# Kernel tuning notes

Measured on AMD Instinct MI355X. Metric: run time of the kernel, lower is better.

Reference implementation:

```python
import jax, jax.numpy as jnp
import numpy as np

B, N, M, H, D = 16, 512, 16, 8, 128  # batch, nodes, neighbors, heads, input_dim
NEG_SLOPE = 0.2
EPS = 1e-5

def _glorot(key, shape):
    fan = sum(shape[-2:]) if len(shape) >= 2 else shape[-1]
    return jax.random.normal(key, shape, dtype=jnp.float32) * (2.0 / fan) ** 0.5

def setup_inputs() -> dict:
    key = jax.random.key(0)
    ks = jax.random.split(key, 12)
    h = jax.random.normal(ks[0], (B, N, D), dtype=jnp.float32)
    adj = jax.random.randint(ks[1], (B, N, M), 0, 2, dtype=jnp.int32)
    n_list = jax.random.randint(ks[2], (B, N, M), 0, N, dtype=jnp.int32)
    W = _glorot(ks[3], (H, D, D))            # per-head projection
    a_src = _glorot(ks[4], (H, D))           # attention vector, source half
    a_dst = _glorot(ks[5], (H, D))           # attention vector, neighbor half
    Wo = _glorot(ks[6], (H * D, D))          # concat-heads output projection
    ln1_g = jnp.ones((D,), jnp.float32); ln1_b = jnp.zeros((D,), jnp.float32)
    ff_w1 = _glorot(ks[7], (D, 2 * D)); ff_b1 = jnp.zeros((2 * D,), jnp.float32)
    ff_w2 = _glorot(ks[8], (2 * D, D)); ff_b2 = jnp.zeros((D,), jnp.float32)
    ln2_g = jnp.ones((D,), jnp.float32); ln2_b = jnp.zeros((D,), jnp.float32)
    return {"h": h, "adj": adj, "n_list": n_list, "W": W, "a_src": a_src,
            "a_dst": a_dst, "Wo": Wo, "ln1_g": ln1_g, "ln1_b": ln1_b,
            "ff_w1": ff_w1, "ff_b1": ff_b1, "ff_w2": ff_w2, "ff_b2": ff_b2,
            "ln2_g": ln2_g, "ln2_b": ln2_b}

def _layer_norm(x, g, b):
    mu = jnp.mean(x, axis=-1, keepdims=True)
    var = jnp.mean(jnp.square(x - mu), axis=-1, keepdims=True)
    return (x - mu) * jax.lax.rsqrt(var + EPS) * g + b

def _gat(h, adj, n_list, W, a_src, a_dst, Wo):
    Wh = jnp.einsum('bnd,hde->bnhe', h, W)                 # [B,N,H,D]
    s_src = jnp.einsum('bnhe,he->bnh', Wh, a_src)          # [B,N,H]
    s_dst = jnp.einsum('bnhe,he->bnh', Wh, a_dst)          # [B,N,H]
    gather = jax.vmap(lambda x, idx: x[idx])               # per-graph gather
    neigh = gather(Wh, n_list)                             # [B,N,M,H,D]
    s_dst_n = gather(s_dst, n_list)                        # [B,N,M,H]
    e = jax.nn.leaky_relu(s_src[:, :, None, :] + s_dst_n, NEG_SLOPE)
    e = jnp.where(adj[..., None] > 0, e, jnp.float32(-1e9))
    attn = jax.nn.softmax(e, axis=2)                       # over M neighbors
    out = jnp.einsum('bnmh,bnmhe->bnhe', attn, neigh)      # [B,N,H,D]
    return out.reshape(out.shape[0], out.shape[1], -1) @ Wo  # [B,N,D]

def reference(h, adj, n_list, W, a_src, a_dst, Wo, ln1_g, ln1_b,
              ff_w1, ff_b1, ff_w2, ff_b2, ln2_g, ln2_b):
    att = _gat(h, adj, n_list, W, a_src, a_dst, Wo)
    t = _layer_norm(att + h, ln1_g, ln1_b)
    ff = jax.nn.relu(t @ ff_w1 + ff_b1) @ ff_w2 + ff_b2
    return _layer_norm(ff + t, ln2_g, ln2_b)
```

## Files before the change

### kernel.cpp

```cpp
#include <hip/hip_runtime.h>
#include <hip/hip_bf16.h>

#define B_  16
#define N_  512
#define M_  16
#define H_  8
#define D_  128
#define BN_ 8192
#define NB  16

typedef __attribute__((ext_vector_type(4))) float          f32x4;
typedef __attribute__((ext_vector_type(4))) _Float16       f16x4;
typedef __attribute__((ext_vector_type(8))) unsigned short u16x8;
typedef __attribute__((ext_vector_type(8))) _Float16       f16x8;

static __device__ __forceinline__ float bf2f(__hip_bfloat16 x) { return __bfloat162float(x); }
static __device__ __forceinline__ unsigned short f2bu(float x) {
    __hip_bfloat16 b = __float2bfloat16(x);
    return *reinterpret_cast<unsigned short*>(&b);
}
static __device__ __forceinline__ float bu2f(unsigned short u) {
    return __uint_as_float(((unsigned int)u) << 16);
}

template <bool F32>
struct Pol {
    static __device__ __forceinline__ float ld(const void* p, int i) {
        if constexpr (F32) return ((const float*)p)[i];
        else               return bf2f(((const __hip_bfloat16*)p)[i]);
    }
    static __device__ __forceinline__ float4 ld4(const void* p, int i) {
        if constexpr (F32) return *(const float4*)((const float*)p + i);
        else {
            const ushort4 u = *(const ushort4*)((const unsigned short*)p + i);
            return make_float4(bu2f(u.x), bu2f(u.y), bu2f(u.z), bu2f(u.w));
        }
    }
    static __device__ __forceinline__ void ld8(const void* p, long i, float* v) {
        if constexpr (F32) {
            const float4 a = *(const float4*)((const float*)p + i);
            const float4 b = *(const float4*)((const float*)p + i + 4);
            v[0]=a.x; v[1]=a.y; v[2]=a.z; v[3]=a.w;
            v[4]=b.x; v[5]=b.y; v[6]=b.z; v[7]=b.w;
        } else {
            const u16x8 u = *(const u16x8*)((const unsigned short*)p + i);
            #pragma unroll
            for (int j = 0; j < 8; ++j) v[j] = bu2f(u[j]);
        }
    }
    static __device__ __forceinline__ void st8(void* p, long i, const float* v) {
        if constexpr (F32) {
            *(float4*)((float*)p + i)     = make_float4(v[0], v[1], v[2], v[3]);
            *(float4*)((float*)p + i + 4) = make_float4(v[4], v[5], v[6], v[7]);
        } else {
            u16x8 u;
            #pragma unroll
            for (int j = 0; j < 8; ++j) u[j] = f2bu(v[j]);
            *(u16x8*)((unsigned short*)p + i) = u;
        }
    }
};

static __device__ __forceinline__ bool probe_is_f32(const void* h) {
    bool is_f32 = false;
    const __hip_bfloat16* hb = (const __hip_bfloat16*)h;
    for (int i = 0; i < 128; ++i) {
        const float v = bf2f(hb[2 * i]);
        if (!(fabsf(v) < 1e4f)) is_f32 = true;
    }
    return is_f32;
}

template <bool F32>
static __device__ __forceinline__ void k0_body(
        const void* __restrict__ W,  const void* __restrict__ Wo,
        const void* __restrict__ a_src, const void* __restrict__ a_dst,
        float* __restrict__ wsrc, float* __restrict__ wdst,
        _Float16* __restrict__ WeffT, float* wrow ) {
    using P = Pol<F32>;
    const int blk = blockIdx.x;
    const int t   = threadIdx.x;
    if (blk < 512) {
        const int half = t >> 7, o = t & 127;
        const int hd = blk * 2 + half;
        wrow[half * 128 + o] = P::ld(W, hd * 128 + o);
        __syncthreads();
        const int hh = hd >> 7;
        float acc = 0.f;
        #pragma unroll 8
        for (int e = 0; e < 128; ++e)
            acc += wrow[half * 128 + e] * P::ld(Wo, (hh * 128 + e) * 128 + o);
        WeffT[(size_t)o * 1024 + hd] = (_Float16)acc;
    } else {
        const int hh = blk - 512;
        const int which = t >> 7, d = t & 127;
        const void* av = which ? a_dst : a_src;
        const int wbase = hh * (D_ * D_) + d * 128;
        float acc = 0.f;
        #pragma unroll 8
        for (int e = 0; e < 128; e += 4) {
            const float4 wv = P::ld4(W, wbase + e);
            const float4 aa = P::ld4(av, hh * 128 + e);
            acc += wv.x * aa.x + wv.y * aa.y + wv.z * aa.z + wv.w * aa.w;
        }
        (which ? wdst : wsrc)[hh * 128 + d] = acc;
    }
}

__global__ __launch_bounds__(256) void k0(
        const void* W, const void* Wo, const void* a_src, const void* a_dst,
        const void* h, float* wsrc, float* wdst, _Float16* WeffT) {
    __shared__ float wrow[2 * 128];
    if (probe_is_f32(h)) k0_body<true >(W, Wo, a_src, a_dst, wsrc, wdst, WeffT, wrow);
    else                 k0_body<false>(W, Wo, a_src, a_dst, wsrc, wdst, WeffT, wrow);
}

template <bool F32>
static __device__ __forceinline__ void k1_body(
        const void* __restrict__ h, const float* __restrict__ wsrc,
        const float* __restrict__ wdst, _Float16* __restrict__ ssrc_h,
        _Float16* __restrict__ sdst_h, float* hls , float* wls ) {
    using P = Pol<F32>;
    const int t   = threadIdx.x;
    const int bn0 = blockIdx.x * 16;
    {
        const int r = t >> 4, c0 = (t & 15) * 8;
        float v[8];
        P::ld8(h, (long)(bn0 + r) * 128 + c0, v);
        #pragma unroll
        for (int j = 0; j < 8; ++j) hls[r * 132 + c0 + j] = v[j];
        const int c = t >> 4;
        const float* wp = (c >> 3) ? wdst : wsrc;
        const int woff = (c & 7) * 128 + c0;
        #pragma unroll
        for (int j = 0; j < 8; ++j) wls[c * 132 + c0 + j] = wp[woff + j];
    }
    __syncthreads();
    const int n = t >> 4, c = t & 15;
    float acc = 0.f;
    #pragma unroll
    for (int e = 0; e < 128; e += 4) {
        const float4 hv = *(const float4*)(hls + n * 132 + e);
        const float4 wv = *(const float4*)(wls + c * 132 + e);
        acc += hv.x * wv.x + hv.y * wv.y + hv.z * wv.z + hv.w * wv.w;
    }
    const int node = bn0 + n;
    if (c < 8) ssrc_h[node * 8 + c]       = (_Float16)acc;
    else       sdst_h[node * 8 + (c - 8)] = (_Float16)acc;
}

__global__ __launch_bounds__(256) void k1(const void* h, const float* wsrc,
                                          const float* wdst, _Float16* ssrc_h,
                                          _Float16* sdst_h) {
    __shared__ float hls[16 * 132];
    __shared__ float wls[16 * 132];
    if (probe_is_f32(h)) k1_body<true >(h, wsrc, wdst, ssrc_h, sdst_h, hls, wls);
    else                 k1_body<false>(h, wsrc, wdst, ssrc_h, sdst_h, hls, wls);
}

struct __align__(16) Smem {
    union {
        _Float16 Zh[NB][1024];
        struct {
            float    ts[NB][132];
            _Float16 us[NB][260];
            float    ys[NB][128];
        } ff;
    } u;
    float hs[NB][128];
    union {
        float attn[NB][16][8];
        float yln[NB][128];
    } v;
    int   nls[NB][16];
    int   adjs[NB][16];
    float ssrc[NB][8];
};

template <bool F32>
static __device__ __forceinline__ void gat_body(
        Smem& s,
        const void* __restrict__ h,
        const int*  __restrict__ adj,
        const int*  __restrict__ n_list,
        const _Float16* __restrict__ ssrc_h,
        const _Float16* __restrict__ sdst_h,
        const _Float16* __restrict__ WeffT,
        const void* __restrict__ g1, const void* __restrict__ bb1,
        const void* __restrict__ w1, const void* __restrict__ fb1,
        const void* __restrict__ w2, const void* __restrict__ fb2,
        const void* __restrict__ g2, const void* __restrict__ bb2,
        void* __restrict__ out) {
    using P = Pol<F32>;
    const int t   = threadIdx.x;
    const int bn0 = blockIdx.x * NB;
    const int b   = bn0 >> 9;
    const int l   = t & 63;
    const int w   = t >> 6;
    const int lo  = l & 15;
    const int hi  = l >> 4;

    {
        const int r = t >> 5, c0 = (t & 31) * 4;
        const float4 v = P::ld4(h, (bn0 + r) * 128 + c0);
        *(float4*)&s.hs[r][c0] = v;
    }
    if (t < 256) {
        const int r = t >> 4, m = t & 15;
        s.nls[r][m]  = n_list[(bn0 + r) * M_ + m] & (N_ - 1);
        s.adjs[r][m] = adj[(bn0 + r) * M_ + m];
    }
    if (t < NB * 8) s.ssrc[t >> 3][t & 7] = (float)ssrc_h[bn0 * 8 + t];
    __syncthreads();

    if (t < 256) {
        const int r = t >> 4, m = t & 15;
        const int nbr = s.nls[r][m];
        const f16x8 sd = *(const f16x8*)(sdst_h + (size_t)(b * N_ + nbr) * 8);
        const int amask = s.adjs[r][m];
        float sc[8];
        #pragma unroll
        for (int hh = 0; hh < 8; ++hh) {
            float x = s.ssrc[r][hh] + (float)sd[hh];
            x = x > 0.f ? x : 0.2f * x;
            if (amask == 0) x = -1e9f;
            sc[hh] = x;
        }
        *(float4*)&s.v.attn[r][m][0] = make_float4(sc[0], sc[1], sc[2], sc[3]);
        *(float4*)&s.v.attn[r][m][4] = make_float4(sc[4], sc[5], sc[6], sc[7]);
    }
    __syncthreads();

    if (t < NB * 8) {
        const int r = t >> 3, hh = t & 7;
        float mx = -3.4e38f;
        #pragma unroll
        for (int m = 0; m < 16; ++m) mx = fmaxf(mx, s.v.attn[r][m][hh]);
        float ex[16], sum = 0.f;
        #pragma unroll
        for (int m = 0; m < 16; ++m) { ex[m] = __expf(s.v.attn[r][m][hh] - mx); sum += ex[m]; }
        const float inv = 1.f / sum;
        #pragma unroll
        for (int m = 0; m < 16; ++m) s.v.attn[r][m][hh] = ex[m] * inv;
    }
    __syncthreads();

    {
        const int r = t >> 5, dc = t & 31, d0 = dc * 4;
        float z[8][4];
        #pragma unroll
        for (int hh = 0; hh < 8; ++hh)
            #pragma unroll
            for (int jj = 0; jj < 4; ++jj) z[hh][jj] = 0.f;
        #pragma unroll 4
        for (int m = 0; m < 16; ++m) {
            const int nbr = s.nls[r][m];
            const float4 hv = P::ld4(h, (b * N_ + nbr) * 128 + d0);
            const float hv4[4] = { hv.x, hv.y, hv.z, hv.w };
            const float4 a0 = *(const float4*)&s.v.attn[r][m][0];
            const float4 a1 = *(const float4*)&s.v.attn[r][m][4];
            const float av[8] = { a0.x, a0.y, a0.z, a0.w, a1.x, a1.y, a1.z, a1.w };
            #pragma unroll
            for (int hh = 0; hh < 8; ++hh)
                #pragma unroll
                for (int jj = 0; jj < 4; ++jj) z[hh][jj] += av[hh] * hv4[jj];
        }
        char* zb = (char*)&s.u.Zh[0][0] + r * 2048;
        const int xo = (r & 7) << 4;
        #pragma unroll
        for (int hh = 0; hh < 8; ++hh) {
            f16x4 vv;
            #pragma unroll
            for (int jj = 0; jj < 4; ++jj) vv[jj] = (_Float16)z[hh][jj];
            *(f16x4*)(zb + ((hh * 256 + dc * 8) ^ xo)) = vv;
        }
    }
    __syncthreads();

    {
        const char* za  = (const char*)&s.u.Zh[0][0] + lo * 2048;
        const int   xo  = (lo & 7) << 4;
        const char* wb0 = (const char*)(WeffT + (size_t)(w * 16 + lo) * 1024);
        f32x4 acc0 = {0.f, 0.f, 0.f, 0.f};
        #pragma unroll 8
        for (int ks = 0; ks < 64; ++ks) {
            const int kb = ks * 32 + hi * 8;
            const f16x4 a  = *(const f16x4*)(za + (kb ^ xo));
            const f16x4 b0 = *(const f16x4*)(wb0 + kb);
            acc0 = __builtin_amdgcn_mfma_f32_16x16x16f16(a, b0, acc0, 0, 0, 0);
        }
        const int o0 = w * 16 + lo;
        #pragma unroll
        for (int q = 0; q < 4; ++q) {
            const int rr = hi * 4 + q;
            s.v.yln[rr][o0] = acc0[q] + s.hs[rr][o0];
        }
    }
    __syncthreads();

    if (t < 256) {
        const int r = t >> 4, j0 = (t & 15) * 8;
        const float4 x0 = *(const float4*)&s.v.yln[r][j0];
        const float4 x1 = *(const float4*)&s.v.yln[r][j0 + 4];
        const float x[8] = { x0.x, x0.y, x0.z, x0.w, x1.x, x1.y, x1.z, x1.w };
        float sm = 0.f, ss = 0.f;
        #pragma unroll
        for (int j = 0; j < 8; ++j) { sm += x[j]; ss += x[j] * x[j]; }
        #pragma unroll
        for (int off = 8; off > 0; off >>= 1) {
            sm += __shfl_xor(sm, off);
            ss += __shfl_xor(ss, off);
        }
        const float mu   = sm * (1.f / 128.f);
        const float var  = ss * (1.f / 128.f) - mu * mu;
        const float rstd = rsqrtf(var + 1e-5f);
        float gv[8], bv[8];
        P::ld8(g1, j0, gv);
        P::ld8(bb1, j0, bv);
        #pragma unroll
        for (int j = 0; j < 8; ++j)
            s.u.ff.ts[r][j0 + j] = (x[j] - mu) * rstd * gv[j] + bv[j];
    }
    __syncthreads();

    {
        f32x4 acc[2] = { {0.f,0.f,0.f,0.f}, {0.f,0.f,0.f,0.f} };
        #pragma unroll
        for (int ks = 0; ks < 8; ++ks) {
            const int k = ks * 16 + hi * 4;
            const float4 tv = *(const float4*)&s.u.ff.ts[lo][k];
            f16x4 a;
            a[0] = (_Float16)tv.x; a[1] = (_Float16)tv.y;
            a[2] = (_Float16)tv.z; a[3] = (_Float16)tv.w;
            #pragma unroll
            for (int nt = 0; nt < 2; ++nt) {
                const int o = w * 32 + nt * 16 + lo;
                f16x4 bb;
                #pragma unroll
                for (int j = 0; j < 4; ++j) bb[j] = (_Float16)P::ld(w1, (k + j) * 256 + o);
                acc[nt] = __builtin_amdgcn_mfma_f32_16x16x16f16(a, bb, acc[nt], 0, 0, 0);
            }
        }
        #pragma unroll
        for (int nt = 0; nt < 2; ++nt) {
            const int o = w * 32 + nt * 16 + lo;
            const float bias = P::ld(fb1, o);
            #pragma unroll
            for (int q = 0; q < 4; ++q)
                s.u.ff.us[hi * 4 + q][o] = (_Float16)fmaxf(acc[nt][q] + bias, 0.f);
        }
    }
    __syncthreads();

    {
        const int o0 = w * 16 + lo;
        f32x4 acc = {0.f, 0.f, 0.f, 0.f};
        #pragma unroll
        for (int ks = 0; ks < 16; ++ks) {
            const int k = ks * 16 + hi * 4;
            const f16x4 a = *(const f16x4*)&s.u.ff.us[lo][k];
            f16x4 bb;
            #pragma unroll
            for (int j = 0; j < 4; ++j) bb[j] = (_Float16)P::ld(w2, (k + j) * 128 + o0);
            acc = __builtin_amdgcn_mfma_f32_16x16x16f16(a, bb, acc, 0, 0, 0);
        }
        const float bias = P::ld(fb2, o0);
        #pragma unroll
        for (int q = 0; q < 4; ++q) {
            const int rr = hi * 4 + q;
            s.u.ff.ys[rr][o0] = acc[q] + bias + s.u.ff.ts[rr][o0];
        }
    }
    __syncthreads();

    if (t < 256) {
        const int r = t >> 4, j0 = (t & 15) * 8;
        const float4 x0 = *(const float4*)&s.u.ff.ys[r][j0];
        const float4 x1 = *(const float4*)&s.u.ff.ys[r][j0 + 4];
        const float x[8] = { x0.x, x0.y, x0.z, x0.w, x1.x, x1.y, x1.z, x1.w };
        float sm = 0.f, ss = 0.f;
        #pragma unroll
        for (int j = 0; j < 8; ++j) { sm += x[j]; ss += x[j] * x[j]; }
        #pragma unroll
        for (int off = 8; off > 0; off >>= 1) {
            sm += __shfl_xor(sm, off);
            ss += __shfl_xor(ss, off);
        }
        const float mu   = sm * (1.f / 128.f);
        const float var  = ss * (1.f / 128.f) - mu * mu;
        const float rstd = rsqrtf(var + 1e-5f);
        float gv[8], bv[8], o8[8];
        P::ld8(g2, j0, gv);
        P::ld8(bb2, j0, bv);
        #pragma unroll
        for (int j = 0; j < 8; ++j) o8[j] = (x[j] - mu) * rstd * gv[j] + bv[j];
        P::st8(out, (long)(bn0 + r) * 128 + j0, o8);
    }
}

__global__ __launch_bounds__(512) void k_gat(
        const void* __restrict__ h,
        const int*  __restrict__ adj,
        const int*  __restrict__ n_list,
        const _Float16* __restrict__ ssrc_h,
        const _Float16* __restrict__ sdst_h,
        const _Float16* __restrict__ WeffT,
        const void* __restrict__ g1, const void* __restrict__ bb1,
        const void* __restrict__ w1, const void* __restrict__ fb1,
        const void* __restrict__ w2, const void* __restrict__ fb2,
        const void* __restrict__ g2, const void* __restrict__ bb2,
        void* __restrict__ out) {
    __shared__ Smem s;
    if (probe_is_f32(h))
        gat_body<true >(s, h, adj, n_list, ssrc_h, sdst_h, WeffT,
                        g1, bb1, w1, fb1, w2, fb2, g2, bb2, out);
    else
        gat_body<false>(s, h, adj, n_list, ssrc_h, sdst_h, WeffT,
                        g1, bb1, w1, fb1, w2, fb2, g2, bb2, out);
}

extern "C" void kernel_launch(void* const* d_in, const int* in_sizes, int n_in,
                              void* d_out, int out_size, void* d_ws, size_t ws_size,
                              hipStream_t stream) {
    (void)in_sizes; (void)n_in; (void)out_size; (void)ws_size;

    char* wsb = (char*)d_ws;
    float*     wsrc  = (float*)(wsb);
    float*     wdst  = (float*)(wsb + 4096);
    _Float16*  ssrc  = (_Float16*)(wsb + 8192);
    _Float16*  sdst  = (_Float16*)(wsb + 139264);
    _Float16*  WeffT = (_Float16*)(wsb + 270336);

    k0<<<520,      256, 0, stream>>>(d_in[3], d_in[6], d_in[4], d_in[5], d_in[0],
                                     wsrc, wdst, WeffT);
    k1<<<BN_ / 16, 256, 0, stream>>>(d_in[0], wsrc, wdst, ssrc, sdst);
    k_gat<<<BN_ / NB, 512, 0, stream>>>(
        d_in[0], (const int*)d_in[1], (const int*)d_in[2], ssrc, sdst, WeffT,
        d_in[7], d_in[8], d_in[9], d_in[10], d_in[11], d_in[12],
        d_in[13], d_in[14], d_out);
}
```

Before: 158.9 us.

## Merge score kernels into one launch and halve nodes per GAT block

Folds the attention-vector projection and per-node score computation into a single kernel. Each score block now recomputes the W·a_src and W·a_dst vectors itself, which removes one launch and its dependency. The main GAT kernel now handles 8 nodes per block instead of 16, which doubles the grid for more parallelism. The MFMA tiles are still 16 rows, so half of each tile is wasted, and the fused kernel repeats the W·a work in all 512 score blocks.

```diff
diff --git a/kernel.cpp b/kernel.cpp
--- a/kernel.cpp
+++ b/kernel.cpp
@@ -7,9 +7,10 @@
 #define H_  8
 #define D_  128
 #define BN_ 8192
-#define NB  16
+#define NB  8
 
 typedef __attribute__((ext_vector_type(4))) float          f32x4;
+typedef __attribute__((ext_vector_type(2))) _Float16       f16x2;
 typedef __attribute__((ext_vector_type(4))) _Float16       f16x4;
 typedef __attribute__((ext_vector_type(8))) unsigned short u16x8;
 typedef __attribute__((ext_vector_type(8))) _Float16       f16x8;
@@ -28,6 +29,13 @@
     static __device__ __forceinline__ float ld(const void* p, int i) {
         if constexpr (F32) return ((const float*)p)[i];
         else               return bf2f(((const __hip_bfloat16*)p)[i]);
+    }
+    static __device__ __forceinline__ float2 ld2(const void* p, long i) {
+        if constexpr (F32) return *(const float2*)((const float*)p + i);
+        else {
+            const ushort2 u = *(const ushort2*)((const unsigned short*)p + i);
+            return make_float2(bu2f(u.x), bu2f(u.y));
+        }
     }
     static __device__ __forceinline__ float4 ld4(const void* p, int i) {
         if constexpr (F32) return *(const float4*)((const float*)p + i);
@@ -72,15 +80,18 @@
 }
 
 template <bool F32>
-static __device__ __forceinline__ void k0_body(
+static __device__ __forceinline__ void kA_body(
         const void* __restrict__ W,  const void* __restrict__ Wo,
         const void* __restrict__ a_src, const void* __restrict__ a_dst,
-        float* __restrict__ wsrc, float* __restrict__ wdst,
-        _Float16* __restrict__ WeffT, float* wrow ) {
+        const void* __restrict__ h,
+        _Float16* __restrict__ WeffT,
+        _Float16* __restrict__ ssrc_h, _Float16* __restrict__ sdst_h,
+        float* sbuf ) {
     using P = Pol<F32>;
     const int blk = blockIdx.x;
     const int t   = threadIdx.x;
     if (blk < 512) {
+        float* wrow = sbuf;
         const int half = t >> 7, o = t & 127;
         const int hd = blk * 2 + half;
         wrow[half * 128 + o] = P::ld(W, hd * 128 + o);
@@ -92,70 +103,59 @@
             acc += wrow[half * 128 + e] * P::ld(Wo, (hh * 128 + e) * 128 + o);
         WeffT[(size_t)o * 1024 + hd] = (_Float16)acc;
     } else {
-        const int hh = blk - 512;
-        const int which = t >> 7, d = t & 127;
-        const void* av = which ? a_dst : a_src;
-        const int wbase = hh * (D_ * D_) + d * 128;
+        float* hls = sbuf;
+        float* wls = sbuf + 16 * 132;
+        const int bn0 = (blk - 512) * 16;
+        {
+            const int r = t >> 4, c0 = (t & 15) * 8;
+            float v[8];
+            P::ld8(h, (long)(bn0 + r) * 128 + c0, v);
+            #pragma unroll
+            for (int j = 0; j < 8; ++j) hls[r * 132 + c0 + j] = v[j];
+        }
+        {
+            const int h_  = t >> 5;
+            const int d00 = (t & 31) * 4;
+            #pragma unroll
+            for (int dd = 0; dd < 4; ++dd) {
+                const int d = d00 + dd;
+                float accS = 0.f, accD = 0.f;
+                for (int e0 = 0; e0 < 128; e0 += 8) {
+                    float wv[8], as[8], ad[8];
+                    P::ld8(W, (long)(h_ * 128 + d) * 128 + e0, wv);
+                    P::ld8(a_src, h_ * 128 + e0, as);
+                    P::ld8(a_dst, h_ * 128 + e0, ad);
+                    #pragma unroll
+                    for (int j = 0; j < 8; ++j) {
+                        accS += wv[j] * as[j];
+                        accD += wv[j] * ad[j];
+                    }
+                }
+                wls[h_ * 132 + d]       = accS;
+                wls[(8 + h_) * 132 + d] = accD;
+            }
+        }
+        __syncthreads();
+        const int n = t >> 4, c = t & 15;
         float acc = 0.f;
-        #pragma unroll 8
+        #pragma unroll
         for (int e = 0; e < 128; e += 4) {
-            const float4 wv = P::ld4(W, wbase + e);
-            const float4 aa = P::ld4(av, hh * 128 + e);
-            acc += wv.x * aa.x + wv.y * aa.y + wv.z * aa.z + wv.w * aa.w;
-        }
-        (which ? wdst : wsrc)[hh * 128 + d] = acc;
-    }
-}
-
-__global__ __launch_bounds__(256) void k0(
+            const float4 hv = *(const float4*)(hls + n * 132 + e);
+            const float4 wv = *(const float4*)(wls + c * 132 + e);
+            acc += hv.x * wv.x + hv.y * wv.y + hv.z * wv.z + hv.w * wv.w;
+        }
+        const int node = bn0 + n;
+        if (c < 8) ssrc_h[node * 8 + c]       = (_Float16)acc;
+        else       sdst_h[node * 8 + (c - 8)] = (_Float16)acc;
+    }
+}
+
+__global__ __launch_bounds__(256) void kA(
         const void* W, const void* Wo, const void* a_src, const void* a_dst,
-        const void* h, float* wsrc, float* wdst, _Float16* WeffT) {
-    __shared__ float wrow[2 * 128];
-    if (probe_is_f32(h)) k0_body<true >(W, Wo, a_src, a_dst, wsrc, wdst, WeffT, wrow);
-    else                 k0_body<false>(W, Wo, a_src, a_dst, wsrc, wdst, WeffT, wrow);
-}
-
-template <bool F32>
-static __device__ __forceinline__ void k1_body(
-        const void* __restrict__ h, const float* __restrict__ wsrc,
-        const float* __restrict__ wdst, _Float16* __restrict__ ssrc_h,
-        _Float16* __restrict__ sdst_h, float* hls , float* wls ) {
-    using P = Pol<F32>;
-    const int t   = threadIdx.x;
-    const int bn0 = blockIdx.x * 16;
-    {
-        const int r = t >> 4, c0 = (t & 15) * 8;
-        float v[8];
-        P::ld8(h, (long)(bn0 + r) * 128 + c0, v);
-        #pragma unroll
-        for (int j = 0; j < 8; ++j) hls[r * 132 + c0 + j] = v[j];
-        const int c = t >> 4;
-        const float* wp = (c >> 3) ? wdst : wsrc;
-        const int woff = (c & 7) * 128 + c0;
-        #pragma unroll
-        for (int j = 0; j < 8; ++j) wls[c * 132 + c0 + j] = wp[woff + j];
-    }
-    __syncthreads();
-    const int n = t >> 4, c = t & 15;
-    float acc = 0.f;
-    #pragma unroll
-    for (int e = 0; e < 128; e += 4) {
-        const float4 hv = *(const float4*)(hls + n * 132 + e);
-        const float4 wv = *(const float4*)(wls + c * 132 + e);
-        acc += hv.x * wv.x + hv.y * wv.y + hv.z * wv.z + hv.w * wv.w;
-    }
-    const int node = bn0 + n;
-    if (c < 8) ssrc_h[node * 8 + c]       = (_Float16)acc;
-    else       sdst_h[node * 8 + (c - 8)] = (_Float16)acc;
-}
-
-__global__ __launch_bounds__(256) void k1(const void* h, const float* wsrc,
-                                          const float* wdst, _Float16* ssrc_h,
-                                          _Float16* sdst_h) {
-    __shared__ float hls[16 * 132];
-    __shared__ float wls[16 * 132];
-    if (probe_is_f32(h)) k1_body<true >(h, wsrc, wdst, ssrc_h, sdst_h, hls, wls);
-    else                 k1_body<false>(h, wsrc, wdst, ssrc_h, sdst_h, hls, wls);
+        const void* h, _Float16* WeffT, _Float16* ssrc_h, _Float16* sdst_h) {
+    __shared__ float sbuf[2 * 16 * 132];
+    if (probe_is_f32(h)) kA_body<true >(W, Wo, a_src, a_dst, h, WeffT, ssrc_h, sdst_h, sbuf);
+    else                 kA_body<false>(W, Wo, a_src, a_dst, h, WeffT, ssrc_h, sdst_h, sbuf);
 }
 
 struct __align__(16) Smem {
@@ -201,19 +201,21 @@
     const int hi  = l >> 4;
 
     {
-        const int r = t >> 5, c0 = (t & 31) * 4;
-        const float4 v = P::ld4(h, (bn0 + r) * 128 + c0);
-        *(float4*)&s.hs[r][c0] = v;
-    }
-    if (t < 256) {
+        const int r = t >> 6, c0 = (t & 63) * 2;
+        const float2 v = P::ld2(h, (long)(bn0 + r) * 128 + c0);
+        *(float2*)&s.hs[r][c0] = v;
+    }
+    if (t < 128) {
         const int r = t >> 4, m = t & 15;
         s.nls[r][m]  = n_list[(bn0 + r) * M_ + m] & (N_ - 1);
         s.adjs[r][m] = adj[(bn0 + r) * M_ + m];
-    }
-    if (t < NB * 8) s.ssrc[t >> 3][t & 7] = (float)ssrc_h[bn0 * 8 + t];
-    __syncthreads();
-
-    if (t < 256) {
+    } else if (t < 128 + NB * 8) {
+        const int i = t - 128;
+        s.ssrc[i >> 3][i & 7] = (float)ssrc_h[bn0 * 8 + i];
+    }
+    __syncthreads();
+
+    if (t < NB * 16) {
         const int r = t >> 4, m = t & 15;
         const int nbr = s.nls[r][m];
         const f16x8 sd = *(const f16x8*)(sdst_h + (size_t)(b * N_ + nbr) * 8);
@@ -246,39 +248,37 @@
     __syncthreads();
 
     {
-        const int r = t >> 5, dc = t & 31, d0 = dc * 4;
-        float z[8][4];
-        #pragma unroll
-        for (int hh = 0; hh < 8; ++hh)
-            #pragma unroll
-            for (int jj = 0; jj < 4; ++jj) z[hh][jj] = 0.f;
+        const int r = t >> 6, dc = t & 63, d0 = dc * 2;
+        float z[8][2];
+        #pragma unroll
+        for (int hh = 0; hh < 8; ++hh) { z[hh][0] = 0.f; z[hh][1] = 0.f; }
         #pragma unroll 4
         for (int m = 0; m < 16; ++m) {
             const int nbr = s.nls[r][m];
-            const float4 hv = P::ld4(h, (b * N_ + nbr) * 128 + d0);
-            const float hv4[4] = { hv.x, hv.y, hv.z, hv.w };
+            const float2 hv = P::ld2(h, (long)(b * N_ + nbr) * 128 + d0);
             const float4 a0 = *(const float4*)&s.v.attn[r][m][0];
             const float4 a1 = *(const float4*)&s.v.attn[r][m][4];
             const float av[8] = { a0.x, a0.y, a0.z, a0.w, a1.x, a1.y, a1.z, a1.w };
             #pragma unroll
-            for (int hh = 0; hh < 8; ++hh)
-                #pragma unroll
-                for (int jj = 0; jj < 4; ++jj) z[hh][jj] += av[hh] * hv4[jj];
+            for (int hh = 0; hh < 8; ++hh) {
+                z[hh][0] += av[hh] * hv.x;
+                z[hh][1] += av[hh] * hv.y;
+            }
         }
         char* zb = (char*)&s.u.Zh[0][0] + r * 2048;
         const int xo = (r & 7) << 4;
         #pragma unroll
         for (int hh = 0; hh < 8; ++hh) {
-            f16x4 vv;
-            #pragma unroll
-            for (int jj = 0; jj < 4; ++jj) vv[jj] = (_Float16)z[hh][jj];
-            *(f16x4*)(zb + ((hh * 256 + dc * 8) ^ xo)) = vv;
+            f16x2 vv;
+            vv[0] = (_Float16)z[hh][0];
+            vv[1] = (_Float16)z[hh][1];
+            *(f16x2*)(zb + ((hh * 256 + dc * 4) ^ xo)) = vv;
         }
     }
     __syncthreads();
 
     {
-        const char* za  = (const char*)&s.u.Zh[0][0] + lo * 2048;
+        const char* za  = (const char*)&s.u.Zh[0][0] + (lo & 7) * 2048;
         const int   xo  = (lo & 7) << 4;
         const char* wb0 = (const char*)(WeffT + (size_t)(w * 16 + lo) * 1024);
         f32x4 acc0 = {0.f, 0.f, 0.f, 0.f};
@@ -289,16 +289,18 @@
             const f16x4 b0 = *(const f16x4*)(wb0 + kb);
             acc0 = __builtin_amdgcn_mfma_f32_16x16x16f16(a, b0, acc0, 0, 0, 0);
         }
-        const int o0 = w * 16 + lo;
-        #pragma unroll
-        for (int q = 0; q < 4; ++q) {
-            const int rr = hi * 4 + q;
-            s.v.yln[rr][o0] = acc0[q] + s.hs[rr][o0];
-        }
-    }
-    __syncthreads();
-
-    if (t < 256) {
+        if (hi < 2) {
+            const int o0 = w * 16 + lo;
+            #pragma unroll
+            for (int q = 0; q < 4; ++q) {
+                const int rr = hi * 4 + q;
+                s.v.yln[rr][o0] = acc0[q] + s.hs[rr][o0];
+            }
+        }
+    }
+    __syncthreads();
+
+    if (t < NB * 16) {
         const int r = t >> 4, j0 = (t & 15) * 8;
         const float4 x0 = *(const float4*)&s.v.yln[r][j0];
         const float4 x1 = *(const float4*)&s.v.yln[r][j0 + 4];
@@ -328,7 +330,7 @@
         #pragma unroll
         for (int ks = 0; ks < 8; ++ks) {
             const int k = ks * 16 + hi * 4;
-            const float4 tv = *(const float4*)&s.u.ff.ts[lo][k];
+            const float4 tv = *(const float4*)&s.u.ff.ts[lo & 7][k];
             f16x4 a;
             a[0] = (_Float16)tv.x; a[1] = (_Float16)tv.y;
             a[2] = (_Float16)tv.z; a[3] = (_Float16)tv.w;
@@ -341,13 +343,15 @@
                 acc[nt] = __builtin_amdgcn_mfma_f32_16x16x16f16(a, bb, acc[nt], 0, 0, 0);
             }
         }
-        #pragma unroll
-        for (int nt = 0; nt < 2; ++nt) {
-            const int o = w * 32 + nt * 16 + lo;
-            const float bias = P::ld(fb1, o);
-            #pragma unroll
-            for (int q = 0; q < 4; ++q)
-                s.u.ff.us[hi * 4 + q][o] = (_Float16)fmaxf(acc[nt][q] + bias, 0.f);
+        if (hi < 2) {
+            #pragma unroll
+            for (int nt = 0; nt < 2; ++nt) {
+                const int o = w * 32 + nt * 16 + lo;
+                const float bias = P::ld(fb1, o);
+                #pragma unroll
+                for (int q = 0; q < 4; ++q)
+                    s.u.ff.us[hi * 4 + q][o] = (_Float16)fmaxf(acc[nt][q] + bias, 0.f);
+            }
         }
     }
     __syncthreads();
@@ -358,22 +362,24 @@
         #pragma unroll
         for (int ks = 0; ks < 16; ++ks) {
             const int k = ks * 16 + hi * 4;
-            const f16x4 a = *(const f16x4*)&s.u.ff.us[lo][k];
+            const f16x4 a = *(const f16x4*)&s.u.ff.us[lo & 7][k];
             f16x4 bb;
             #pragma unroll
             for (int j = 0; j < 4; ++j) bb[j] = (_Float16)P::ld(w2, (k + j) * 128 + o0);
             acc = __builtin_amdgcn_mfma_f32_16x16x16f16(a, bb, acc, 0, 0, 0);
         }
-        const float bias = P::ld(fb2, o0);
-        #pragma unroll
-        for (int q = 0; q < 4; ++q) {
-            const int rr = hi * 4 + q;
-            s.u.ff.ys[rr][o0] = acc[q] + bias + s.u.ff.ts[rr][o0];
-        }
-    }
-    __syncthreads();
-
-    if (t < 256) {
+        if (hi < 2) {
+            const float bias = P::ld(fb2, o0);
+            #pragma unroll
+            for (int q = 0; q < 4; ++q) {
+                const int rr = hi * 4 + q;
+                s.u.ff.ys[rr][o0] = acc[q] + bias + s.u.ff.ts[rr][o0];
+            }
+        }
+    }
+    __syncthreads();
+
+    if (t < NB * 16) {
         const int r = t >> 4, j0 = (t & 15) * 8;
         const float4 x0 = *(const float4*)&s.u.ff.ys[r][j0];
         const float4 x1 = *(const float4*)&s.u.ff.ys[r][j0 + 4];
@@ -425,15 +431,12 @@
     (void)in_sizes; (void)n_in; (void)out_size; (void)ws_size;
 
     char* wsb = (char*)d_ws;
-    float*     wsrc  = (float*)(wsb);
-    float*     wdst  = (float*)(wsb + 4096);
     _Float16*  ssrc  = (_Float16*)(wsb + 8192);
     _Float16*  sdst  = (_Float16*)(wsb + 139264);
     _Float16*  WeffT = (_Float16*)(wsb + 270336);
 
-    k0<<<520,      256, 0, stream>>>(d_in[3], d_in[6], d_in[4], d_in[5], d_in[0],
-                                     wsrc, wdst, WeffT);
-    k1<<<BN_ / 16, 256, 0, stream>>>(d_in[0], wsrc, wdst, ssrc, sdst);
+    kA<<<1024, 256, 0, stream>>>(d_in[3], d_in[6], d_in[4], d_in[5], d_in[0],
+                                 WeffT, ssrc, sdst);
     k_gat<<<BN_ / NB, 512, 0, stream>>>(
         d_in[0], (const int*)d_in[1], (const int*)d_in[2], ssrc, sdst, WeffT,
         d_in[7], d_in[8], d_in[9], d_in[10], d_in[11], d_in[12],
```

Measured after the change: 227.4 us. 1.43x slower.

## Double GAT block to 1024 threads with split-K GEMMs and partial-sum reduction

Applied to the files above, without the earlier changes.

Raises the fused GAT kernel from 512 to 1024 threads per block. The aggregation phase now gives each thread 2 output columns instead of 4. The Wo and FF2 GEMMs are split along K across two wave groups, and their partial sums go through a new shared buffer plus an extra reduction pass. FF1 now gives each wave one 16-column tile instead of two. The aim is more parallelism and latency hiding per block. The cost is extra syncs, more shared memory, and possibly lower occupancy or register limits at 1024 threads.

```diff
diff --git a/kernel.cpp b/kernel.cpp
--- a/kernel.cpp
+++ b/kernel.cpp
@@ -10,6 +10,7 @@
 #define NB  16
 
 typedef __attribute__((ext_vector_type(4))) float          f32x4;
+typedef __attribute__((ext_vector_type(2))) _Float16       f16x2;
 typedef __attribute__((ext_vector_type(4))) _Float16       f16x4;
 typedef __attribute__((ext_vector_type(8))) unsigned short u16x8;
 typedef __attribute__((ext_vector_type(8))) _Float16       f16x8;
@@ -28,6 +29,13 @@
     static __device__ __forceinline__ float ld(const void* p, int i) {
         if constexpr (F32) return ((const float*)p)[i];
         else               return bf2f(((const __hip_bfloat16*)p)[i]);
+    }
+    static __device__ __forceinline__ float2 ld2(const void* p, long i) {
+        if constexpr (F32) return *(const float2*)((const float*)p + i);
+        else {
+            const ushort2 u = *(const ushort2*)((const unsigned short*)p + i);
+            return make_float2(bu2f(u.x), bu2f(u.y));
+        }
     }
     static __device__ __forceinline__ float4 ld4(const void* p, int i) {
         if constexpr (F32) return *(const float4*)((const float*)p + i);
@@ -167,6 +175,7 @@
             float    ys[NB][128];
         } ff;
     } u;
+    float part[NB][128];
     float hs[NB][128];
     union {
         float attn[NB][16][8];
@@ -199,21 +208,25 @@
     const int w   = t >> 6;
     const int lo  = l & 15;
     const int hi  = l >> 4;
-
-    {
-        const int r = t >> 5, c0 = (t & 31) * 4;
-        const float4 v = P::ld4(h, (bn0 + r) * 128 + c0);
-        *(float4*)&s.hs[r][c0] = v;
+    const int wo  = w & 7;
+    const int kh  = w >> 3;
+
+    {
+        const int r = t >> 6, c0 = (t & 63) * 2;
+        const float2 v = P::ld2(h, (long)(bn0 + r) * 128 + c0);
+        *(float2*)&s.hs[r][c0] = v;
     }
     if (t < 256) {
         const int r = t >> 4, m = t & 15;
         s.nls[r][m]  = n_list[(bn0 + r) * M_ + m] & (N_ - 1);
         s.adjs[r][m] = adj[(bn0 + r) * M_ + m];
-    }
-    if (t < NB * 8) s.ssrc[t >> 3][t & 7] = (float)ssrc_h[bn0 * 8 + t];
-    __syncthreads();
-
-    if (t < 256) {
+    } else if (t < 256 + NB * 8) {
+        const int i = t - 256;
+        s.ssrc[i >> 3][i & 7] = (float)ssrc_h[bn0 * 8 + i];
+    }
+    __syncthreads();
+
+    if (t < NB * 16) {
         const int r = t >> 4, m = t & 15;
         const int nbr = s.nls[r][m];
         const f16x8 sd = *(const f16x8*)(sdst_h + (size_t)(b * N_ + nbr) * 8);
@@ -246,33 +259,31 @@
     __syncthreads();
 
     {
-        const int r = t >> 5, dc = t & 31, d0 = dc * 4;
-        float z[8][4];
-        #pragma unroll
-        for (int hh = 0; hh < 8; ++hh)
-            #pragma unroll
-            for (int jj = 0; jj < 4; ++jj) z[hh][jj] = 0.f;
+        const int r = t >> 6, dc = t & 63, d0 = dc * 2;
+        float z[8][2];
+        #pragma unroll
+        for (int hh = 0; hh < 8; ++hh) { z[hh][0] = 0.f; z[hh][1] = 0.f; }
         #pragma unroll 4
         for (int m = 0; m < 16; ++m) {
             const int nbr = s.nls[r][m];
-            const float4 hv = P::ld4(h, (b * N_ + nbr) * 128 + d0);
-            const float hv4[4] = { hv.x, hv.y, hv.z, hv.w };
+            const float2 hv = P::ld2(h, (long)(b * N_ + nbr) * 128 + d0);
             const float4 a0 = *(const float4*)&s.v.attn[r][m][0];
             const float4 a1 = *(const float4*)&s.v.attn[r][m][4];
             const float av[8] = { a0.x, a0.y, a0.z, a0.w, a1.x, a1.y, a1.z, a1.w };
             #pragma unroll
-            for (int hh = 0; hh < 8; ++hh)
-                #pragma unroll
-                for (int jj = 0; jj < 4; ++jj) z[hh][jj] += av[hh] * hv4[jj];
+            for (int hh = 0; hh < 8; ++hh) {
+                z[hh][0] += av[hh] * hv.x;
+                z[hh][1] += av[hh] * hv.y;
+            }
         }
         char* zb = (char*)&s.u.Zh[0][0] + r * 2048;
         const int xo = (r & 7) << 4;
         #pragma unroll
         for (int hh = 0; hh < 8; ++hh) {
-            f16x4 vv;
-            #pragma unroll
-            for (int jj = 0; jj < 4; ++jj) vv[jj] = (_Float16)z[hh][jj];
-            *(f16x4*)(zb + ((hh * 256 + dc * 8) ^ xo)) = vv;
+            f16x2 vv;
+            vv[0] = (_Float16)z[hh][0];
+            vv[1] = (_Float16)z[hh][1];
+            *(f16x2*)(zb + ((hh * 256 + dc * 4) ^ xo)) = vv;
         }
     }
     __syncthreads();
@@ -280,25 +291,35 @@
     {
         const char* za  = (const char*)&s.u.Zh[0][0] + lo * 2048;
         const int   xo  = (lo & 7) << 4;
-        const char* wb0 = (const char*)(WeffT + (size_t)(w * 16 + lo) * 1024);
+        const char* wb0 = (const char*)(WeffT + (size_t)(wo * 16 + lo) * 1024) + kh * 1024;
         f32x4 acc0 = {0.f, 0.f, 0.f, 0.f};
         #pragma unroll 8
-        for (int ks = 0; ks < 64; ++ks) {
-            const int kb = ks * 32 + hi * 8;
-            const f16x4 a  = *(const f16x4*)(za + (kb ^ xo));
+        for (int ks = 0; ks < 32; ++ks) {
+            const int kb  = ks * 32 + hi * 8;
+            const f16x4 a  = *(const f16x4*)(za + ((kh * 1024 + kb) ^ xo));
             const f16x4 b0 = *(const f16x4*)(wb0 + kb);
             acc0 = __builtin_amdgcn_mfma_f32_16x16x16f16(a, b0, acc0, 0, 0, 0);
         }
-        const int o0 = w * 16 + lo;
+        const int o0 = wo * 16 + lo;
         #pragma unroll
         for (int q = 0; q < 4; ++q) {
             const int rr = hi * 4 + q;
-            s.v.yln[rr][o0] = acc0[q] + s.hs[rr][o0];
-        }
-    }
-    __syncthreads();
-
-    if (t < 256) {
+            if (kh == 0) s.v.yln[rr][o0] = acc0[q] + s.hs[rr][o0];
+            else         s.part[rr][o0]  = acc0[q];
+        }
+    }
+    __syncthreads();
+    {
+        const int i = t * 2;
+        float* yp = &s.v.yln[0][0];
+        const float2 pv = *(const float2*)(&s.part[0][0] + i);
+        float2 yv = *(const float2*)(yp + i);
+        yv.x += pv.x; yv.y += pv.y;
+        *(float2*)(yp + i) = yv;
+    }
+    __syncthreads();
+
+    if (t < NB * 16) {
         const int r = t >> 4, j0 = (t & 15) * 8;
         const float4 x0 = *(const float4*)&s.v.yln[r][j0];
         const float4 x1 = *(const float4*)&s.v.yln[r][j0 + 4];
@@ -324,7 +345,8 @@
     __syncthreads();
 
     {
-        f32x4 acc[2] = { {0.f,0.f,0.f,0.f}, {0.f,0.f,0.f,0.f} };
+        const int o = w * 16 + lo;
+        f32x4 acc = {0.f, 0.f, 0.f, 0.f};
         #pragma unroll
         for (int ks = 0; ks < 8; ++ks) {
             const int k = ks * 16 + hi * 4;
@@ -332,32 +354,24 @@
             f16x4 a;
             a[0] = (_Float16)tv.x; a[1] = (_Float16)tv.y;
             a[2] = (_Float16)tv.z; a[3] = (_Float16)tv.w;
+            f16x4 bb;
             #pragma unroll
-            for (int nt = 0; nt < 2; ++nt) {
-                const int o = w * 32 + nt * 16 + lo;
-                f16x4 bb;
-                #pragma unroll
-                for (int j = 0; j < 4; ++j) bb[j] = (_Float16)P::ld(w1, (k + j) * 256 + o);
-                acc[nt] = __builtin_amdgcn_mfma_f32_16x16x16f16(a, bb, acc[nt], 0, 0, 0);
-            }
-        }
-        #pragma unroll
-        for (int nt = 0; nt < 2; ++nt) {
-            const int o = w * 32 + nt * 16 + lo;
-            const float bias = P::ld(fb1, o);
-            #pragma unroll
-            for (int q = 0; q < 4; ++q)
-                s.u.ff.us[hi * 4 + q][o] = (_Float16)fmaxf(acc[nt][q] + bias, 0.f);
-        }
-    }
-    __syncthreads();
-
-    {
-        const int o0 = w * 16 + lo;
+            for (int j = 0; j < 4; ++j) bb[j] = (_Float16)P::ld(w1, (k + j) * 256 + o);
+            acc = __builtin_amdgcn_mfma_f32_16x16x16f16(a, bb, acc, 0, 0, 0);
+        }
+        const float bias = P::ld(fb1, o);
+        #pragma unroll
+        for (int q = 0; q < 4; ++q)
+            s.u.ff.us[hi * 4 + q][o] = (_Float16)fmaxf(acc[q] + bias, 0.f);
+    }
+    __syncthreads();
+
+    {
+        const int o0 = wo * 16 + lo;
         f32x4 acc = {0.f, 0.f, 0.f, 0.f};
         #pragma unroll
-        for (int ks = 0; ks < 16; ++ks) {
-            const int k = ks * 16 + hi * 4;
+        for (int ks = 0; ks < 8; ++ks) {
+            const int k = kh * 128 + ks * 16 + hi * 4;
             const f16x4 a = *(const f16x4*)&s.u.ff.us[lo][k];
             f16x4 bb;
             #pragma unroll
@@ -368,12 +382,22 @@
         #pragma unroll
         for (int q = 0; q < 4; ++q) {
             const int rr = hi * 4 + q;
-            s.u.ff.ys[rr][o0] = acc[q] + bias + s.u.ff.ts[rr][o0];
-        }
-    }
-    __syncthreads();
-
-    if (t < 256) {
+            if (kh == 0) s.u.ff.ys[rr][o0] = acc[q] + bias + s.u.ff.ts[rr][o0];
+            else         s.part[rr][o0]    = acc[q];
+        }
+    }
+    __syncthreads();
+    {
+        const int i = t * 2;
+        float* yp = &s.u.ff.ys[0][0];
+        const float2 pv = *(const float2*)(&s.part[0][0] + i);
+        float2 yv = *(const float2*)(yp + i);
+        yv.x += pv.x; yv.y += pv.y;
+        *(float2*)(yp + i) = yv;
+    }
+    __syncthreads();
+
+    if (t < NB * 16) {
         const int r = t >> 4, j0 = (t & 15) * 8;
         const float4 x0 = *(const float4*)&s.u.ff.ys[r][j0];
         const float4 x1 = *(const float4*)&s.u.ff.ys[r][j0 + 4];
@@ -398,7 +422,7 @@
     }
 }
 
-__global__ __launch_bounds__(512) void k_gat(
+__global__ __launch_bounds__(1024) void k_gat(
         const void* __restrict__ h,
         const int*  __restrict__ adj,
         const int*  __restrict__ n_list,
@@ -434,7 +458,7 @@
     k0<<<520,      256, 0, stream>>>(d_in[3], d_in[6], d_in[4], d_in[5], d_in[0],
                                      wsrc, wdst, WeffT);
     k1<<<BN_ / 16, 256, 0, stream>>>(d_in[0], wsrc, wdst, ssrc, sdst);
-    k_gat<<<BN_ / NB, 512, 0, stream>>>(
+    k_gat<<<BN_ / NB, 1024, 0, stream>>>(
         d_in[0], (const int*)d_in[1], (const int*)d_in[2], ssrc, sdst, WeffT,
         d_in[7], d_in[8], d_in[9], d_in[10], d_in[11], d_in[12],
         d_in[13], d_in[14], d_out);
```

New measurement: 161.1 us. Within noise of the previous version (+1.4%).

## Pre-transpose FFN weights to fp16 and merge setup kernels

Applied to the files above, without the earlier changes.

Splits the attention-vector precompute into its own small kernel. It merges the WeffT build, the per-node score computation and new fp16 transposes of ff_w1/ff_w2 into one kernel, so launches go from three to three but with reshuffled dependencies. The main kernel then preloads the transposed weight fragments into registers as vector loads, replacing scalar strided global loads with conversion inside the MFMA loops. It adds launch_bounds occupancy hints and a fallback path when the workspace is too small, at the cost of more registers held per thread.

```diff
diff --git a/kernel.cpp b/kernel.cpp
--- a/kernel.cpp
+++ b/kernel.cpp
@@ -10,6 +10,7 @@
 #define NB  16
 
 typedef __attribute__((ext_vector_type(4))) float          f32x4;
+typedef __attribute__((ext_vector_type(2))) _Float16       f16x2;
 typedef __attribute__((ext_vector_type(4))) _Float16       f16x4;
 typedef __attribute__((ext_vector_type(8))) unsigned short u16x8;
 typedef __attribute__((ext_vector_type(8))) _Float16       f16x8;
@@ -28,6 +29,13 @@
     static __device__ __forceinline__ float ld(const void* p, int i) {
         if constexpr (F32) return ((const float*)p)[i];
         else               return bf2f(((const __hip_bfloat16*)p)[i]);
+    }
+    static __device__ __forceinline__ float2 ld2(const void* p, long i) {
+        if constexpr (F32) return *(const float2*)((const float*)p + i);
+        else {
+            const ushort2 u = *(const ushort2*)((const unsigned short*)p + i);
+            return make_float2(bu2f(u.x), bu2f(u.y));
+        }
     }
     static __device__ __forceinline__ float4 ld4(const void* p, int i) {
         if constexpr (F32) return *(const float4*)((const float*)p + i);
@@ -72,15 +80,48 @@
 }
 
 template <bool F32>
-static __device__ __forceinline__ void k0_body(
+static __device__ __forceinline__ void k0s_body(
+        const void* __restrict__ W, const void* __restrict__ a_src,
+        const void* __restrict__ a_dst,
+        float* __restrict__ wsrc, float* __restrict__ wdst) {
+    using P = Pol<F32>;
+    const int hh = blockIdx.x;
+    const int t  = threadIdx.x;
+    const int which = t >> 7, d = t & 127;
+    const void* av = which ? a_dst : a_src;
+    const int wbase = hh * (D_ * D_) + d * 128;
+    float acc = 0.f;
+    #pragma unroll 8
+    for (int e = 0; e < 128; e += 4) {
+        const float4 wv = P::ld4(W, wbase + e);
+        const float4 aa = P::ld4(av, hh * 128 + e);
+        acc += wv.x * aa.x + wv.y * aa.y + wv.z * aa.z + wv.w * aa.w;
+    }
+    (which ? wdst : wsrc)[hh * 128 + d] = acc;
+}
+
+__global__ __launch_bounds__(256) void k0s(
+        const void* W, const void* a_src, const void* a_dst, const void* h,
+        float* wsrc, float* wdst) {
+    if (probe_is_f32(h)) k0s_body<true >(W, a_src, a_dst, wsrc, wdst);
+    else                 k0s_body<false>(W, a_src, a_dst, wsrc, wdst);
+}
+
+template <bool F32>
+static __device__ __forceinline__ void kB_body(
         const void* __restrict__ W,  const void* __restrict__ Wo,
-        const void* __restrict__ a_src, const void* __restrict__ a_dst,
-        float* __restrict__ wsrc, float* __restrict__ wdst,
-        _Float16* __restrict__ WeffT, float* wrow ) {
+        const void* __restrict__ h,
+        const float* __restrict__ wsrc, const float* __restrict__ wdst,
+        const void* __restrict__ w1, const void* __restrict__ w2,
+        _Float16* __restrict__ WeffT,
+        _Float16* __restrict__ ssrc_h, _Float16* __restrict__ sdst_h,
+        _Float16* __restrict__ w1T, _Float16* __restrict__ w2T,
+        float* sbuf ) {
     using P = Pol<F32>;
     const int blk = blockIdx.x;
     const int t   = threadIdx.x;
     if (blk < 512) {
+        float* wrow = sbuf;
         const int half = t >> 7, o = t & 127;
         const int hd = blk * 2 + half;
         wrow[half * 128 + o] = P::ld(W, hd * 128 + o);
@@ -91,71 +132,64 @@
         for (int e = 0; e < 128; ++e)
             acc += wrow[half * 128 + e] * P::ld(Wo, (hh * 128 + e) * 128 + o);
         WeffT[(size_t)o * 1024 + hd] = (_Float16)acc;
+    } else if (blk < 1024) {
+        float* hls = sbuf;
+        float* wls = sbuf + 16 * 132;
+        const int bn0 = (blk - 512) * 16;
+        {
+            const int r = t >> 4, c0 = (t & 15) * 8;
+            float v[8];
+            P::ld8(h, (long)(bn0 + r) * 128 + c0, v);
+            #pragma unroll
+            for (int j = 0; j < 8; ++j) hls[r * 132 + c0 + j] = v[j];
+            const int c = t >> 4;
+            const float* wp = (c >> 3) ? wdst : wsrc;
+            const int woff = (c & 7) * 128 + c0;
+            #pragma unroll
+            for (int j = 0; j < 8; ++j) wls[c * 132 + c0 + j] = wp[woff + j];
+        }
+        __syncthreads();
+        const int n = t >> 4, c = t & 15;
+        float acc = 0.f;
+        #pragma unroll
+        for (int e = 0; e < 128; e += 4) {
+            const float4 hv = *(const float4*)(hls + n * 132 + e);
+            const float4 wv = *(const float4*)(wls + c * 132 + e);
+            acc += hv.x * wv.x + hv.y * wv.y + hv.z * wv.z + hv.w * wv.w;
+        }
+        const int node = bn0 + n;
+        if (c < 8) ssrc_h[node * 8 + c]       = (_Float16)acc;
+        else       sdst_h[node * 8 + (c - 8)] = (_Float16)acc;
+    } else if (blk == 1024) {
+        const int o = t;
+        for (int k0 = 0; k0 < 128; k0 += 8) {
+            f16x8 v;
+            #pragma unroll
+            for (int j = 0; j < 8; ++j) v[j] = (_Float16)P::ld(w1, (k0 + j) * 256 + o);
+            *(f16x8*)(w1T + o * 128 + k0) = v;
+        }
     } else {
-        const int hh = blk - 512;
-        const int which = t >> 7, d = t & 127;
-        const void* av = which ? a_dst : a_src;
-        const int wbase = hh * (D_ * D_) + d * 128;
-        float acc = 0.f;
-        #pragma unroll 8
-        for (int e = 0; e < 128; e += 4) {
-            const float4 wv = P::ld4(W, wbase + e);
-            const float4 aa = P::ld4(av, hh * 128 + e);
-            acc += wv.x * aa.x + wv.y * aa.y + wv.z * aa.z + wv.w * aa.w;
-        }
-        (which ? wdst : wsrc)[hh * 128 + d] = acc;
-    }
-}
-
-__global__ __launch_bounds__(256) void k0(
-        const void* W, const void* Wo, const void* a_src, const void* a_dst,
-        const void* h, float* wsrc, float* wdst, _Float16* WeffT) {
-    __shared__ float wrow[2 * 128];
-    if (probe_is_f32(h)) k0_body<true >(W, Wo, a_src, a_dst, wsrc, wdst, WeffT, wrow);
-    else                 k0_body<false>(W, Wo, a_src, a_dst, wsrc, wdst, WeffT, wrow);
-}
-
-template <bool F32>
-static __device__ __forceinline__ void k1_body(
-        const void* __restrict__ h, const float* __restrict__ wsrc,
-        const float* __restrict__ wdst, _Float16* __restrict__ ssrc_h,
-        _Float16* __restrict__ sdst_h, float* hls , float* wls ) {
-    using P = Pol<F32>;
-    const int t   = threadIdx.x;
-    const int bn0 = blockIdx.x * 16;
-    {
-        const int r = t >> 4, c0 = (t & 15) * 8;
-        float v[8];
-        P::ld8(h, (long)(bn0 + r) * 128 + c0, v);
-        #pragma unroll
-        for (int j = 0; j < 8; ++j) hls[r * 132 + c0 + j] = v[j];
-        const int c = t >> 4;
-        const float* wp = (c >> 3) ? wdst : wsrc;
-        const int woff = (c & 7) * 128 + c0;
-        #pragma unroll
-        for (int j = 0; j < 8; ++j) wls[c * 132 + c0 + j] = wp[woff + j];
-    }
-    __syncthreads();
-    const int n = t >> 4, c = t & 15;
-    float acc = 0.f;
-    #pragma unroll
-    for (int e = 0; e < 128; e += 4) {
-        const float4 hv = *(const float4*)(hls + n * 132 + e);
-        const float4 wv = *(const float4*)(wls + c * 132 + e);
-        acc += hv.x * wv.x + hv.y * wv.y + hv.z * wv.z + hv.w * wv.w;
-    }
-    const int node = bn0 + n;
-    if (c < 8) ssrc_h[node * 8 + c]       = (_Float16)acc;
-    else       sdst_h[node * 8 + (c - 8)] = (_Float16)acc;
-}
-
-__global__ __launch_bounds__(256) void k1(const void* h, const float* wsrc,
-                                          const float* wdst, _Float16* ssrc_h,
-                                          _Float16* sdst_h) {
-    __shared__ float hls[16 * 132];
-    __shared__ float wls[16 * 132];
-    if (probe_is_f32(h)) k1_body<true >(h, wsrc, wdst, ssrc_h, sdst_h, hls, wls);
-    else                 k1_body<false>(h, wsrc, wdst, ssrc_h, sdst_h, hls, wls);
+        const int o = t & 127, kh = t >> 7;
+        for (int k0 = kh * 128; k0 < kh * 128 + 128; k0 += 8) {
+            f16x8 v;
+            #pragma unroll
+            for (int j = 0; j < 8; ++j) v[j] = (_Float16)P::ld(w2, (k0 + j) * 128 + o);
+            *(f16x8*)(w2T + o * 256 + k0) = v;
+        }
+    }
+}
+
+__global__ __launch_bounds__(256) void kB(
+        const void* W, const void* Wo, const void* h,
+        const float* wsrc, const float* wdst,
+        const void* w1, const void* w2,
+        _Float16* WeffT, _Float16* ssrc_h, _Float16* sdst_h,
+        _Float16* w1T, _Float16* w2T) {
+    __shared__ float sbuf[2 * 16 * 132];
+    if (probe_is_f32(h))
+        kB_body<true >(W, Wo, h, wsrc, wdst, w1, w2, WeffT, ssrc_h, sdst_h, w1T, w2T, sbuf);
+    else
+        kB_body<false>(W, Wo, h, wsrc, wdst, w1, w2, WeffT, ssrc_h, sdst_h, w1T, w2T, sbuf);
 }
 
 struct __align__(16) Smem {
@@ -177,7 +211,7 @@
     float ssrc[NB][8];
 };
 
-template <bool F32>
+template <bool F32, bool TW>
 static __device__ __forceinline__ void gat_body(
         Smem& s,
         const void* __restrict__ h,
@@ -186,6 +220,8 @@
         const _Float16* __restrict__ ssrc_h,
         const _Float16* __restrict__ sdst_h,
         const _Float16* __restrict__ WeffT,
+        const _Float16* __restrict__ w1T,
+        const _Float16* __restrict__ w2T,
         const void* __restrict__ g1, const void* __restrict__ bb1,
         const void* __restrict__ w1, const void* __restrict__ fb1,
         const void* __restrict__ w2, const void* __restrict__ fb2,
@@ -277,6 +313,20 @@
     }
     __syncthreads();
 
+    f16x4 pb1[8][2];
+    f16x4 pb2[16];
+    if constexpr (TW) {
+        #pragma unroll
+        for (int ks = 0; ks < 8; ++ks)
+            #pragma unroll
+            for (int nt = 0; nt < 2; ++nt)
+                pb1[ks][nt] = *(const f16x4*)(w1T + (size_t)(w * 32 + nt * 16 + lo) * 128
+                                              + ks * 16 + hi * 4);
+        #pragma unroll
+        for (int ks = 0; ks < 16; ++ks)
+            pb2[ks] = *(const f16x4*)(w2T + (size_t)(w * 16 + lo) * 256 + ks * 16 + hi * 4);
+    }
+
     {
         const char* za  = (const char*)&s.u.Zh[0][0] + lo * 2048;
         const int   xo  = (lo & 7) << 4;
@@ -298,7 +348,7 @@
     }
     __syncthreads();
 
-    if (t < 256) {
+    if (t < NB * 16) {
         const int r = t >> 4, j0 = (t & 15) * 8;
         const float4 x0 = *(const float4*)&s.v.yln[r][j0];
         const float4 x1 = *(const float4*)&s.v.yln[r][j0 + 4];
@@ -334,20 +384,26 @@
             a[2] = (_Float16)tv.z; a[3] = (_Float16)tv.w;
             #pragma unroll
             for (int nt = 0; nt < 2; ++nt) {
-                const int o = w * 32 + nt * 16 + lo;
                 f16x4 bb;
-                #pragma unroll
-                for (int j = 0; j < 4; ++j) bb[j] = (_Float16)P::ld(w1, (k + j) * 256 + o);
+                if constexpr (TW) {
+                    bb = pb1[ks][nt];
+                } else {
+                    const int o = w * 32 + nt * 16 + lo;
+                    #pragma unroll
+                    for (int j = 0; j < 4; ++j) bb[j] = (_Float16)P::ld(w1, (k + j) * 256 + o);
+                }
                 acc[nt] = __builtin_amdgcn_mfma_f32_16x16x16f16(a, bb, acc[nt], 0, 0, 0);
             }
         }
-        #pragma unroll
-        for (int nt = 0; nt < 2; ++nt) {
-            const int o = w * 32 + nt * 16 + lo;
-            const float bias = P::ld(fb1, o);
-            #pragma unroll
-            for (int q = 0; q < 4; ++q)
-                s.u.ff.us[hi * 4 + q][o] = (_Float16)fmaxf(acc[nt][q] + bias, 0.f);
+        if (hi < 4) {
+            #pragma unroll
+            for (int nt = 0; nt < 2; ++nt) {
+                const int o = w * 32 + nt * 16 + lo;
+                const float bias = P::ld(fb1, o);
+                #pragma unroll
+                for (int q = 0; q < 4; ++q)
+                    s.u.ff.us[hi * 4 + q][o] = (_Float16)fmaxf(acc[nt][q] + bias, 0.f);
+            }
         }
     }
     __syncthreads();
@@ -360,8 +416,12 @@
             const int k = ks * 16 + hi * 4;
             const f16x4 a = *(const f16x4*)&s.u.ff.us[lo][k];
             f16x4 bb;
-            #pragma unroll
-            for (int j = 0; j < 4; ++j) bb[j] = (_Float16)P::ld(w2, (k + j) * 128 + o0);
+            if constexpr (TW) {
+                bb = pb2[ks];
+            } else {
+                #pragma unroll
+                for (int j = 0; j < 4; ++j) bb[j] = (_Float16)P::ld(w2, (k + j) * 128 + o0);
+            }
             acc = __builtin_amdgcn_mfma_f32_16x16x16f16(a, bb, acc, 0, 0, 0);
         }
         const float bias = P::ld(fb2, o0);
@@ -373,7 +433,7 @@
     }
     __syncthreads();
 
-    if (t < 256) {
+    if (t < NB * 16) {
         const int r = t >> 4, j0 = (t & 15) * 8;
         const float4 x0 = *(const float4*)&s.u.ff.ys[r][j0];
         const float4 x1 = *(const float4*)&s.u.ff.ys[r][j0 + 4];
@@ -398,13 +458,16 @@
     }
 }
 
-__global__ __launch_bounds__(512) void k_gat(
+template <bool TW>
+__global__ __launch_bounds__(512, 4) void k_gat(
         const void* __restrict__ h,
         const int*  __restrict__ adj,
         const int*  __restrict__ n_list,
         const _Float16* __restrict__ ssrc_h,
         const _Float16* __restrict__ sdst_h,
         const _Float16* __restrict__ WeffT,
+        const _Float16* __restrict__ w1T,
+        const _Float16* __restrict__ w2T,
         const void* __restrict__ g1, const void* __restrict__ bb1,
         const void* __restrict__ w1, const void* __restrict__ fb1,
         const void* __restrict__ w2, const void* __restrict__ fb2,
@@ -412,17 +475,17 @@
         void* __restrict__ out) {
     __shared__ Smem s;
     if (probe_is_f32(h))
-        gat_body<true >(s, h, adj, n_list, ssrc_h, sdst_h, WeffT,
-                        g1, bb1, w1, fb1, w2, fb2, g2, bb2, out);
+        gat_body<true , TW>(s, h, adj, n_list, ssrc_h, sdst_h, WeffT, w1T, w2T,
+                            g1, bb1, w1, fb1, w2, fb2, g2, bb2, out);
     else
-        gat_body<false>(s, h, adj, n_list, ssrc_h, sdst_h, WeffT,
-                        g1, bb1, w1, fb1, w2, fb2, g2, bb2, out);
+        gat_body<false, TW>(s, h, adj, n_list, ssrc_h, sdst_h, WeffT, w1T, w2T,
+                            g1, bb1, w1, fb1, w2, fb2, g2, bb2, out);
 }
 
 extern "C" void kernel_launch(void* const* d_in, const int* in_sizes, int n_in,
                               void* d_out, int out_size, void* d_ws, size_t ws_size,
                               hipStream_t stream) {
-    (void)in_sizes; (void)n_in; (void)out_size; (void)ws_size;
+    (void)in_sizes; (void)n_in; (void)out_size;
 
     char* wsb = (char*)d_ws;
     float*     wsrc  = (float*)(wsb);
@@ -430,12 +493,25 @@
     _Float16*  ssrc  = (_Float16*)(wsb + 8192);
     _Float16*  sdst  = (_Float16*)(wsb + 139264);
     _Float16*  WeffT = (_Float16*)(wsb + 270336);
-
-    k0<<<520,      256, 0, stream>>>(d_in[3], d_in[6], d_in[4], d_in[5], d_in[0],
-                                     wsrc, wdst, WeffT);
-    k1<<<BN_ / 16, 256, 0, stream>>>(d_in[0], wsrc, wdst, ssrc, sdst);
-    k_gat<<<BN_ / NB, 512, 0, stream>>>(
-        d_in[0], (const int*)d_in[1], (const int*)d_in[2], ssrc, sdst, WeffT,
-        d_in[7], d_in[8], d_in[9], d_in[10], d_in[11], d_in[12],
-        d_in[13], d_in[14], d_out);
-}
+    _Float16*  w1T   = (_Float16*)(wsb + 532480);
+    _Float16*  w2T   = (_Float16*)(wsb + 598016);
+
+    const bool big = ws_size >= 663552;
+
+    k0s<<<8, 256, 0, stream>>>(d_in[3], d_in[4], d_in[5], d_in[0], wsrc, wdst);
+    kB<<<big ? 1026 : 1024, 256, 0, stream>>>(
+        d_in[3], d_in[6], d_in[0], wsrc, wdst, d_in[9], d_in[11],
+        WeffT, ssrc, sdst, w1T, w2T);
+    if (big)
+        k_gat<true ><<<BN_ / NB, 512, 0, stream>>>(
+            d_in[0], (const int*)d_in[1], (const int*)d_in[2], ssrc, sdst,
+            WeffT, w1T, w2T,
+            d_in[7], d_in[8], d_in[9], d_in[10], d_in[11], d_in[12],
+            d_in[13], d_in[14], d_out);
+    else
+        k_gat<false><<<BN_ / NB, 512, 0, stream>>>(
+            d_in[0], (const int*)d_in[1], (const int*)d_in[2], ssrc, sdst,
+            WeffT, w1T, w2T,
+            d_in[7], d_in[8], d_in[9], d_in[10], d_in[11], d_in[12],
+            d_in[13], d_in[14], d_out);
+}
```

New measurement: 172.3 us. 1.08x slower.
